# Optimization experiments

Hardware: AMD Instinct MI355X
Metric: run time of the kernel (lower is better)

Reference implementation:

```python
import jax, jax.numpy as jnp
import numpy as np

E = 8
DIMS = [512, 1024, 1024, 512]
BATCH = 2048


def _init_w(key, shape):
    a = np.sqrt(6.0 / (shape[-2] * shape[-1]))
    return jax.random.uniform(key, shape, dtype=jnp.float32, minval=-a, maxval=a)


def setup_inputs() -> dict:
    key = jax.random.key(0)
    ks = jax.random.split(key, 8)
    inp = {
        "weight_blend": jax.random.uniform(ks[0], (BATCH, E), dtype=jnp.float32),
        "x": jax.random.normal(ks[1], (BATCH, DIMS[0]), dtype=jnp.float32),
    }
    for i in range(3):
        inp[f"W{i}"] = _init_w(ks[2 + i], (E, DIMS[i + 1], DIMS[i]))
        inp[f"B{i}"] = jnp.zeros((E, DIMS[i + 1], 1), dtype=jnp.float32)
    return inp


def reference(weight_blend, x, W0, B0, W1, B1, W2, B2):
    Ws = [W0, W1, W2]
    Bs = [B0, B1, B2]
    acts = [jax.nn.elu, jax.nn.elu, None]
    for W, B, act in zip(Ws, Bs, acts):
        # dropout p=0 -> identity
        # blended-expert GEMM: sum_e wb[b,e] * (W[e] @ x[b]) == einsum
        t = jnp.einsum("be,eoi,bi->bo", weight_blend, W, x)
        bias = jnp.einsum("be,eo->bo", weight_blend, B[..., 0])
        x = t + bias
        if act is not None:
            x = act(x)
    return x
```

## Files before the change

### kernel.cpp

```cpp
#include <hip/hip_runtime.h>
#include <math.h>

typedef __attribute__((ext_vector_type(8))) short bf16x8;
typedef __attribute__((ext_vector_type(4))) float f32x4;

#define NEXP 8
#define BATCH 2048

__device__ __forceinline__ unsigned short f2bf(float f) {
    union { float f; unsigned u; } v; v.f = f;
    unsigned r = v.u + 0x7FFFu + ((v.u >> 16) & 1u);
    return (unsigned short)(r >> 16);
}

__global__ __launch_bounds__(256) void pack_all(
    const float* __restrict__ W0, const float* __restrict__ W1,
    const float* __restrict__ W2, const float* __restrict__ x,
    unsigned short* __restrict__ W0p, unsigned short* __restrict__ W1p,
    unsigned short* __restrict__ W2p, unsigned short* __restrict__ x0p)
{
    __shared__ float T[128 * 36];
    const int bid = blockIdx.x, t = threadIdx.x;

    if (bid < 10240) {
        const float* W; unsigned short* out; int KB, Din, Dout, U, lin;
        if (bid < 2048)      { W = W0; out = W0p; KB = 16; Din = 512;  Dout = 1024; U = 4; lin = bid; }
        else if (bid < 6144) { W = W1; out = W1p; KB = 32; Din = 1024; Dout = 1024; U = 4; lin = bid - 2048; }
        else                 { W = W2; out = W2p; KB = 32; Din = 1024; Dout = 512;  U = 2; lin = bid - 6144; }
        const int e  = lin & 7;
        const int r  = lin >> 3;
        const int kb = r % KB;
        const int nb = r / KB;
        const int N0 = nb * 16 * U;
        const int K0 = kb * 32;
        for (int it = 0; it < U / 2; ++it) {
            const int idx = t + 256 * it;
            const int nl = idx >> 3, k4 = (idx & 7) * 4;
            float4 v = *(const float4*)(W + ((size_t)e * Dout + N0 + nl) * Din + K0 + k4);
            *(float4*)(T + nl * 36 + k4) = v;
        }
        __syncthreads();
        if (t < 64 * U) {
            const int u = t >> 6, l = t & 63;
            const float* p = T + (u * 16 + (l & 15)) * 36 + (l >> 4) * 8;
            bf16x8 h;
            #pragma unroll
            for (int j = 0; j < 8; ++j) h[j] = (short)f2bf(p[j]);
            *(bf16x8*)(out + (size_t)lin * (U * 512) + t * 8) = h;
        }
    } else {
        const int lin = bid - 10240;
        const int kb = lin & 15, mb = lin >> 4;
        for (int it = 0; it < 4; ++it) {
            const int idx = t + 256 * it;
            const int ml = idx >> 3, k4 = (idx & 7) * 4;
            float4 v = *(const float4*)(x + (size_t)(mb * 128 + ml) * 512 + kb * 32 + k4);
            *(float4*)(T + ml * 36 + k4) = v;
        }
        __syncthreads();
        #pragma unroll
        for (int it = 0; it < 2; ++it) {
            const int s = t + 256 * it;
            const int g = s >> 6, l = s & 63;
            const float* p = T + (g * 16 + (l & 15)) * 36 + (l >> 4) * 8;
            bf16x8 h;
            #pragma unroll
            for (int j = 0; j < 8; ++j) h[j] = (short)f2bf(p[j]);
            *(bf16x8*)(x0p + (size_t)lin * 4096 + s * 8) = h;
        }
    }
}

template<int NU>
__global__ __launch_bounds__(512, 2) void moe_mfma5(
    const unsigned short* __restrict__ Xp,
    const unsigned short* __restrict__ Wp,
    const float* __restrict__ Bias,
    const float* __restrict__ WBl,
    void* __restrict__ Yout,
    int KB, int Dout, int KBn, int act, int packed_out)
{
    constexpr int BN   = 16 * NU;
    constexpr int PSTR = BN + 4;
    __shared__ __align__(16) float lds_f[2 * 32 * PSTR];

    const int tid = threadIdx.x;
    const int w   = tid >> 6;
    const int l   = tid & 63;
    const int lh  = l >> 4;
    const int ll  = l & 15;
    const int mw  = w & 1;
    const int ew  = w >> 1;
    const int e0  = 2 * ew;
    const int by  = blockIdx.y;
    const int bx  = blockIdx.x;
    const int m0  = by * 128;
    const int n0  = bx * BN;

    f32x4 acc0[4][NU], acc1[4][NU];
    #pragma unroll
    for (int t = 0; t < 4; ++t)
        #pragma unroll
        for (int u = 0; u < NU; ++u)
            #pragma unroll
            for (int i = 0; i < 4; ++i) { acc0[t][u][i] = 0.f; acc1[t][u][i] = 0.f; }

    unsigned aoff[4], boff0[NU], boff1[NU];
    #pragma unroll
    for (int t = 0; t < 4; ++t)
        aoff[t] = ((unsigned)(by * KB) * 8 + mw * 4 + t) * 1024u + l * 16u;
    #pragma unroll
    for (int u = 0; u < NU; ++u) {
        boff0[u] = ((unsigned)(bx * KB) * (8 * NU) + e0 * NU + u) * 1024u + l * 16u;
        boff1[u] = boff0[u] + NU * 1024u;
    }
    const char* xc = (const char*)Xp;
    const char* wc = (const char*)Wp;

    bf16x8 aR[2][4], b0R[2][NU], b1R[2][NU];

    auto LOAD = [&](int s, int kk) {
        const unsigned ab = (unsigned)kk * 8192u;
        const unsigned bb = (unsigned)kk * (8192u * NU);
        #pragma unroll
        for (int t = 0; t < 4; ++t)
            aR[s][t] = *(const bf16x8*)(xc + aoff[t] + ab);
        #pragma unroll
        for (int u = 0; u < NU; ++u) {
            b0R[s][u] = *(const bf16x8*)(wc + boff0[u] + bb);
            b1R[s][u] = *(const bf16x8*)(wc + boff1[u] + bb);
        }
    };
    auto MF = [&](int s) {
        #pragma unroll
        for (int u = 0; u < NU; ++u)
            #pragma unroll
            for (int t = 0; t < 4; ++t) {
                acc0[t][u] = __builtin_amdgcn_mfma_f32_16x16x32_bf16(aR[s][t], b0R[s][u], acc0[t][u], 0, 0, 0);
                acc1[t][u] = __builtin_amdgcn_mfma_f32_16x16x32_bf16(aR[s][t], b1R[s][u], acc1[t][u], 0, 0, 0);
            }
    };

    LOAD(0, 0);
    for (int kk = 0; kk < KB; kk += 2) {
        if (kk + 1 < KB) LOAD(1, kk + 1);
        MF(0);
        if (kk + 2 < KB) LOAD(0, kk + 2);
        MF(1);
    }

    float bi0[NU], bi1[NU];
    #pragma unroll
    for (int u = 0; u < NU; ++u) {
        const int n = n0 + u * 16 + ll;
        bi0[u] = Bias[(size_t)e0 * Dout + n];
        bi1[u] = Bias[(size_t)(e0 + 1) * Dout + n];
    }

    float* pb0 = lds_f;
    float* pb1 = lds_f + 32 * PSTR;
    float* pb  = (ew & 2) ? pb1 : pb0;

    #pragma unroll
    for (int tc = 0; tc < 4; ++tc) {
        __syncthreads();
        if (!(ew & 1)) {
            #pragma unroll
            for (int r = 0; r < 4; ++r) {
                const int lm = 16 * mw + 4 * lh + r;
                const int m  = m0 + 64 * mw + 16 * tc + 4 * lh + r;
                float2 wbp = ((const float2*)(WBl + (size_t)m * NEXP))[ew];
                #pragma unroll
                for (int u = 0; u < NU; ++u)
                    pb[lm * PSTR + u * 16 + ll] =
                        wbp.x * (acc0[tc][u][r] + bi0[u]) + wbp.y * (acc1[tc][u][r] + bi1[u]);
            }
        }
        __syncthreads();
        if (ew & 1) {
            #pragma unroll
            for (int r = 0; r < 4; ++r) {
                const int lm = 16 * mw + 4 * lh + r;
                const int m  = m0 + 64 * mw + 16 * tc + 4 * lh + r;
                float2 wbp = ((const float2*)(WBl + (size_t)m * NEXP))[ew];
                #pragma unroll
                for (int u = 0; u < NU; ++u)
                    pb[lm * PSTR + u * 16 + ll] +=
                        wbp.x * (acc0[tc][u][r] + bi0[u]) + wbp.y * (acc1[tc][u][r] + bi1[u]);
            }
        }
        __syncthreads();
        if (packed_out) {
            const int s = tid;
            if (s < NU * 64) {
                const int kb_loc = s >> 7;
                const int mwq    = (s >> 6) & 1;
                const int sl     = s & 63;
                const int lm     = mwq * 16 + (sl & 15);
                const int c0     = kb_loc * 32 + (sl >> 4) * 8;
                bf16x8 h;
                #pragma unroll
                for (int j = 0; j < 8; ++j) {
                    float v = pb0[lm * PSTR + c0 + j] + pb1[lm * PSTR + c0 + j];
                    v = v > 0.f ? v : expm1f(v);
                    h[j] = (short)f2bf(v);
                }
                const unsigned dst =
                    (((unsigned)by * KBn + (n0 >> 5) + kb_loc) * 8 + mwq * 4 + tc) * 1024u
                    + (unsigned)sl * 16u;
                *(bf16x8*)((char*)Yout + dst) = h;
            }
        } else {
            for (int idx = tid; idx < 32 * BN / 4; idx += 512) {
                const int row = idx / (BN / 4);
                const int c4  = (idx % (BN / 4)) * 4;
                float4 sv = *(const float4*)(pb0 + row * PSTR + c4);
                float4 qv = *(const float4*)(pb1 + row * PSTR + c4);
                sv.x += qv.x; sv.y += qv.y; sv.z += qv.z; sv.w += qv.w;
                if (act) {
                    sv.x = sv.x > 0.f ? sv.x : expm1f(sv.x);
                    sv.y = sv.y > 0.f ? sv.y : expm1f(sv.y);
                    sv.z = sv.z > 0.f ? sv.z : expm1f(sv.z);
                    sv.w = sv.w > 0.f ? sv.w : expm1f(sv.w);
                }
                const int m = m0 + 64 * (row >> 4) + 16 * tc + (row & 15);
                *(float4*)((float*)Yout + (size_t)m * Dout + n0 + c4) = sv;
            }
        }
    }
}

#define BM 64
#define BNF 64
#define BKF 16
#define PAD 4

__global__ __launch_bounds__(256) void moe_layer_f32(
    const float* __restrict__ X, const float* __restrict__ W,
    const float* __restrict__ Bias, const float* __restrict__ WB,
    float* __restrict__ Y, int Din, int Dout, int act)
{
    __shared__ float As[BKF][BM + PAD];
    __shared__ float Bs[BKF][BNF + PAD];
    const int tid = threadIdx.x;
    const int tm = tid >> 4, tn = tid & 15;
    const int m0 = blockIdx.y * BM, n0 = blockIdx.x * BNF;
    const int lr = tid >> 2, lc = (tid & 3) << 2;
    float acc[4][4] = {};
    const float* xrow  = X  + (size_t)(m0 + lr) * Din;
    const float* wbrow = WB + (size_t)(m0 + lr) * NEXP;
    const float* wrow0 = W  + (size_t)(n0 + lr) * Din;
    for (int e = 0; e < NEXP; ++e) {
        const float wbe = wbrow[e];
        const float* wrow = wrow0 + (size_t)e * Dout * Din;
        for (int k0 = 0; k0 < Din; k0 += BKF) {
            float4 av = *(const float4*)(xrow + k0 + lc);
            float4 bv = *(const float4*)(wrow + k0 + lc);
            __syncthreads();
            As[lc+0][lr] = av.x*wbe; As[lc+1][lr] = av.y*wbe;
            As[lc+2][lr] = av.z*wbe; As[lc+3][lr] = av.w*wbe;
            Bs[lc+0][lr] = bv.x; Bs[lc+1][lr] = bv.y;
            Bs[lc+2][lr] = bv.z; Bs[lc+3][lr] = bv.w;
            __syncthreads();
            #pragma unroll
            for (int k = 0; k < BKF; ++k) {
                float4 a = *(const float4*)&As[k][tm << 2];
                float4 b = *(const float4*)&Bs[k][tn << 2];
                acc[0][0]+=a.x*b.x; acc[0][1]+=a.x*b.y; acc[0][2]+=a.x*b.z; acc[0][3]+=a.x*b.w;
                acc[1][0]+=a.y*b.x; acc[1][1]+=a.y*b.y; acc[1][2]+=a.y*b.z; acc[1][3]+=a.y*b.w;
                acc[2][0]+=a.z*b.x; acc[2][1]+=a.z*b.y; acc[2][2]+=a.z*b.z; acc[2][3]+=a.z*b.w;
                acc[3][0]+=a.w*b.x; acc[3][1]+=a.w*b.y; acc[3][2]+=a.w*b.z; acc[3][3]+=a.w*b.w;
            }
        }
    }
    #pragma unroll
    for (int im = 0; im < 4; ++im) {
        const int m = m0 + (tm << 2) + im;
        const float* wbm = WB + (size_t)m * NEXP;
        float wv[NEXP];
        #pragma unroll
        for (int e = 0; e < NEXP; ++e) wv[e] = wbm[e];
        #pragma unroll
        for (int in = 0; in < 4; ++in) {
            const int n = n0 + (tn << 2) + in;
            float bsum = 0.f;
            #pragma unroll
            for (int e = 0; e < NEXP; ++e) bsum += wv[e] * Bias[(size_t)e * Dout + n];
            float v = acc[im][in] + bsum;
            if (act) v = v > 0.f ? v : expm1f(v);
            acc[im][in] = v;
        }
        float4 o = make_float4(acc[im][0], acc[im][1], acc[im][2], acc[im][3]);
        *(float4*)(Y + (size_t)m * Dout + n0 + (tn << 2)) = o;
    }
}

extern "C" void kernel_launch(void* const* d_in, const int* in_sizes, int n_in,
                              void* d_out, int out_size, void* d_ws, size_t ws_size,
                              hipStream_t stream)
{
    (void)in_sizes; (void)n_in; (void)out_size;
    const float* wb = (const float*)d_in[0];
    const float* x  = (const float*)d_in[1];
    const float* W0 = (const float*)d_in[2];
    const float* B0 = (const float*)d_in[3];
    const float* W1 = (const float*)d_in[4];
    const float* B1 = (const float*)d_in[5];
    const float* W2 = (const float*)d_in[6];
    const float* B2 = (const float*)d_in[7];
    float* out = (float*)d_out;

    const size_t NW0 = (size_t)8*1024*512, NW1 = (size_t)8*1024*1024, NW2 = (size_t)8*512*1024;
    const size_t NX0 = (size_t)BATCH*512, NX1 = (size_t)BATCH*1024;
    const size_t need = (NW0 + NW1 + NW2 + NX0 + 2 * NX1) * 2;

    if (ws_size >= need) {
        unsigned short* W0p = (unsigned short*)d_ws;
        unsigned short* W1p = W0p + NW0;
        unsigned short* W2p = W1p + NW1;
        unsigned short* x0p = W2p + NW2;
        unsigned short* x1p = x0p + NX0;
        unsigned short* x2p = x1p + NX1;
        pack_all<<<10496, 256, 0, stream>>>(W0, W1, W2, x, W0p, W1p, W2p, x0p);
        moe_mfma5<4><<<dim3(16, 16), 512, 0, stream>>>(x0p, W0p, B0, wb, x1p, 16, 1024, 32, 1, 1);
        moe_mfma5<4><<<dim3(16, 16), 512, 0, stream>>>(x1p, W1p, B1, wb, x2p, 32, 1024, 32, 1, 1);
        moe_mfma5<2><<<dim3(16, 16), 512, 0, stream>>>(x2p, W2p, B2, wb, out, 32, 512,  0, 0, 0);
    } else {
        float* x1 = (float*)d_ws;
        float* x2 = x1 + (size_t)BATCH * 1024;
        moe_layer_f32<<<dim3(1024/BNF, BATCH/BM), 256, 0, stream>>>(x,  W0, B0, wb, x1, 512,  1024, 1);
        moe_layer_f32<<<dim3(1024/BNF, BATCH/BM), 256, 0, stream>>>(x1, W1, B1, wb, x2, 1024, 1024, 1);
        moe_layer_f32<<<dim3(512/BNF,  BATCH/BM), 256, 0, stream>>>(x2, W2, B2, wb, out, 1024, 512,  0);
    }
}
```

Baseline: 202.3 us.

## Shrink MFMA GEMM tiles to 64x32 with 256 threads for more blocks

Replaces the 512-thread, 128xBN-tile blended-expert GEMM kernel with a 256-thread kernel that computes 64x32 output tiles, each wave owning two experts across all rows. This quadruples the grid (1024 blocks for the 1024-wide layers) so more CUs are busy, and collapses the four-pass LDS reduction epilogue into one two-phase pass. The trade-off is less reuse of each loaded weight and activation fragment per block, so more global/L2 traffic per FLOP.

```diff
diff --git a/kernel.cpp b/kernel.cpp
--- a/kernel.cpp
+++ b/kernel.cpp
@@ -71,8 +71,8 @@
     }
 }
 
-template<int NU>
-__global__ __launch_bounds__(512, 2) void moe_mfma5(
+template<int UP>
+__global__ __launch_bounds__(256, 3) void moe_mfma6(
     const unsigned short* __restrict__ Xp,
     const unsigned short* __restrict__ Wp,
     const float* __restrict__ Bias,
@@ -80,60 +80,64 @@
     void* __restrict__ Yout,
     int KB, int Dout, int KBn, int act, int packed_out)
 {
-    constexpr int BN   = 16 * NU;
-    constexpr int PSTR = BN + 4;
-    __shared__ __align__(16) float lds_f[2 * 32 * PSTR];
-
-    const int tid = threadIdx.x;
-    const int w   = tid >> 6;
-    const int l   = tid & 63;
-    const int lh  = l >> 4;
-    const int ll  = l & 15;
-    const int mw  = w & 1;
-    const int ew  = w >> 1;
-    const int e0  = 2 * ew;
-    const int by  = blockIdx.y;
-    const int bx  = blockIdx.x;
-    const int m0  = by * 128;
-    const int n0  = bx * BN;
-
-    f32x4 acc0[4][NU], acc1[4][NU];
+    constexpr int PSTR = 36;
+    __shared__ __align__(16) float lds_f[2 * 64 * PSTR];
+
+    const int tid  = threadIdx.x;
+    const int ew   = tid >> 6;
+    const int l    = tid & 63;
+    const int lh   = l >> 4;
+    const int ll   = l & 15;
+    const int e0   = 2 * ew;
+    const int bx   = blockIdx.x;
+    const int by   = blockIdx.y;
+    const int m0   = by * 64;
+    const int n0   = bx * 32;
+    const int mb   = by >> 1;
+    const int half = by & 1;
+
+    f32x4 acc0[4][2], acc1[4][2];
     #pragma unroll
     for (int t = 0; t < 4; ++t)
         #pragma unroll
-        for (int u = 0; u < NU; ++u)
+        for (int u = 0; u < 2; ++u)
             #pragma unroll
             for (int i = 0; i < 4; ++i) { acc0[t][u][i] = 0.f; acc1[t][u][i] = 0.f; }
 
-    unsigned aoff[4], boff0[NU], boff1[NU];
+    unsigned aoff[4];
     #pragma unroll
     for (int t = 0; t < 4; ++t)
-        aoff[t] = ((unsigned)(by * KB) * 8 + mw * 4 + t) * 1024u + l * 16u;
-    #pragma unroll
-    for (int u = 0; u < NU; ++u) {
-        boff0[u] = ((unsigned)(bx * KB) * (8 * NU) + e0 * NU + u) * 1024u + l * 16u;
-        boff1[u] = boff0[u] + NU * 1024u;
-    }
+        aoff[t] = (unsigned)(mb * KB) * 8192u + (unsigned)(half * 4 + t) * 1024u + l * 16u;
+    const int nb   = (bx * 2) / UP;
+    const int uoff = (bx * 2) % UP;
+    unsigned boff0[2], boff1[2];
+    #pragma unroll
+    for (int u = 0; u < 2; ++u) {
+        boff0[u] = (((unsigned)(nb * KB) * 8 + e0) * UP + uoff + u) * 1024u + l * 16u;
+        boff1[u] = boff0[u] + UP * 1024u;
+    }
+    const unsigned astr = 8192u;
+    const unsigned bstr = UP * 8192u;
     const char* xc = (const char*)Xp;
     const char* wc = (const char*)Wp;
 
-    bf16x8 aR[2][4], b0R[2][NU], b1R[2][NU];
+    bf16x8 aR[2][4], b0R[2][2], b1R[2][2];
 
     auto LOAD = [&](int s, int kk) {
-        const unsigned ab = (unsigned)kk * 8192u;
-        const unsigned bb = (unsigned)kk * (8192u * NU);
+        const unsigned ab = (unsigned)kk * astr;
+        const unsigned bb = (unsigned)kk * bstr;
         #pragma unroll
         for (int t = 0; t < 4; ++t)
             aR[s][t] = *(const bf16x8*)(xc + aoff[t] + ab);
         #pragma unroll
-        for (int u = 0; u < NU; ++u) {
+        for (int u = 0; u < 2; ++u) {
             b0R[s][u] = *(const bf16x8*)(wc + boff0[u] + bb);
             b1R[s][u] = *(const bf16x8*)(wc + boff1[u] + bb);
         }
     };
     auto MF = [&](int s) {
         #pragma unroll
-        for (int u = 0; u < NU; ++u)
+        for (int u = 0; u < 2; ++u)
             #pragma unroll
             for (int t = 0; t < 4; ++t) {
                 acc0[t][u] = __builtin_amdgcn_mfma_f32_16x16x32_bf16(aR[s][t], b0R[s][u], acc0[t][u], 0, 0, 0);
@@ -149,83 +153,77 @@
         MF(1);
     }
 
-    float bi0[NU], bi1[NU];
-    #pragma unroll
-    for (int u = 0; u < NU; ++u) {
+    float bi0[2], bi1[2];
+    #pragma unroll
+    for (int u = 0; u < 2; ++u) {
         const int n = n0 + u * 16 + ll;
         bi0[u] = Bias[(size_t)e0 * Dout + n];
         bi1[u] = Bias[(size_t)(e0 + 1) * Dout + n];
     }
 
+    float* pb = lds_f + (ew & 1) * (64 * PSTR);
+
+    if (ew < 2) {
+        #pragma unroll
+        for (int t = 0; t < 4; ++t)
+            #pragma unroll
+            for (int r = 0; r < 4; ++r) {
+                const int lm = 16 * t + 4 * lh + r;
+                float2 wbp = ((const float2*)(WBl + (size_t)(m0 + lm) * NEXP))[ew];
+                #pragma unroll
+                for (int u = 0; u < 2; ++u)
+                    pb[lm * PSTR + u * 16 + ll] =
+                        wbp.x * (acc0[t][u][r] + bi0[u]) + wbp.y * (acc1[t][u][r] + bi1[u]);
+            }
+    }
+    __syncthreads();
+    if (ew >= 2) {
+        #pragma unroll
+        for (int t = 0; t < 4; ++t)
+            #pragma unroll
+            for (int r = 0; r < 4; ++r) {
+                const int lm = 16 * t + 4 * lh + r;
+                float2 wbp = ((const float2*)(WBl + (size_t)(m0 + lm) * NEXP))[ew];
+                #pragma unroll
+                for (int u = 0; u < 2; ++u)
+                    pb[lm * PSTR + u * 16 + ll] +=
+                        wbp.x * (acc0[t][u][r] + bi0[u]) + wbp.y * (acc1[t][u][r] + bi1[u]);
+            }
+    }
+    __syncthreads();
+
     float* pb0 = lds_f;
-    float* pb1 = lds_f + 32 * PSTR;
-    float* pb  = (ew & 2) ? pb1 : pb0;
-
-    #pragma unroll
-    for (int tc = 0; tc < 4; ++tc) {
-        __syncthreads();
-        if (!(ew & 1)) {
-            #pragma unroll
-            for (int r = 0; r < 4; ++r) {
-                const int lm = 16 * mw + 4 * lh + r;
-                const int m  = m0 + 64 * mw + 16 * tc + 4 * lh + r;
-                float2 wbp = ((const float2*)(WBl + (size_t)m * NEXP))[ew];
-                #pragma unroll
-                for (int u = 0; u < NU; ++u)
-                    pb[lm * PSTR + u * 16 + ll] =
-                        wbp.x * (acc0[tc][u][r] + bi0[u]) + wbp.y * (acc1[tc][u][r] + bi1[u]);
-            }
-        }
-        __syncthreads();
-        if (ew & 1) {
-            #pragma unroll
-            for (int r = 0; r < 4; ++r) {
-                const int lm = 16 * mw + 4 * lh + r;
-                const int m  = m0 + 64 * mw + 16 * tc + 4 * lh + r;
-                float2 wbp = ((const float2*)(WBl + (size_t)m * NEXP))[ew];
-                #pragma unroll
-                for (int u = 0; u < NU; ++u)
-                    pb[lm * PSTR + u * 16 + ll] +=
-                        wbp.x * (acc0[tc][u][r] + bi0[u]) + wbp.y * (acc1[tc][u][r] + bi1[u]);
-            }
-        }
-        __syncthreads();
-        if (packed_out) {
-            const int s = tid;
-            if (s < NU * 64) {
-                const int kb_loc = s >> 7;
-                const int mwq    = (s >> 6) & 1;
-                const int sl     = s & 63;
-                const int lm     = mwq * 16 + (sl & 15);
-                const int c0     = kb_loc * 32 + (sl >> 4) * 8;
-                bf16x8 h;
-                #pragma unroll
-                for (int j = 0; j < 8; ++j) {
-                    float v = pb0[lm * PSTR + c0 + j] + pb1[lm * PSTR + c0 + j];
-                    v = v > 0.f ? v : expm1f(v);
-                    h[j] = (short)f2bf(v);
-                }
-                const unsigned dst =
-                    (((unsigned)by * KBn + (n0 >> 5) + kb_loc) * 8 + mwq * 4 + tc) * 1024u
-                    + (unsigned)sl * 16u;
-                *(bf16x8*)((char*)Yout + dst) = h;
-            }
-        } else {
-            for (int idx = tid; idx < 32 * BN / 4; idx += 512) {
-                const int row = idx / (BN / 4);
-                const int c4  = (idx % (BN / 4)) * 4;
-                float4 sv = *(const float4*)(pb0 + row * PSTR + c4);
-                float4 qv = *(const float4*)(pb1 + row * PSTR + c4);
-                sv.x += qv.x; sv.y += qv.y; sv.z += qv.z; sv.w += qv.w;
-                if (act) {
-                    sv.x = sv.x > 0.f ? sv.x : expm1f(sv.x);
-                    sv.y = sv.y > 0.f ? sv.y : expm1f(sv.y);
-                    sv.z = sv.z > 0.f ? sv.z : expm1f(sv.z);
-                    sv.w = sv.w > 0.f ? sv.w : expm1f(sv.w);
-                }
-                const int m = m0 + 64 * (row >> 4) + 16 * tc + (row & 15);
-                *(float4*)((float*)Yout + (size_t)m * Dout + n0 + c4) = sv;
-            }
+    float* pb1 = lds_f + 64 * PSTR;
+    if (packed_out) {
+        const int g  = tid >> 6;
+        const int c0 = lh * 8;
+        const int rowbase = (g * 16 + ll) * PSTR;
+        bf16x8 h;
+        #pragma unroll
+        for (int j = 0; j < 8; ++j) {
+            float v = pb0[rowbase + c0 + j] + pb1[rowbase + c0 + j];
+            if (act) v = v > 0.f ? v : expm1f(v);
+            h[j] = (short)f2bf(v);
+        }
+        unsigned short* dst = (unsigned short*)Yout +
+            ((size_t)(mb * KBn + bx) * 8 + half * 4 + g) * 512 + l * 8;
+        *(bf16x8*)dst = h;
+    } else {
+        #pragma unroll
+        for (int it = 0; it < 2; ++it) {
+            const int idx = tid + 256 * it;
+            const int row = idx >> 3;
+            const int c4  = (idx & 7) * 4;
+            float4 s = *(const float4*)(pb0 + row * PSTR + c4);
+            float4 q = *(const float4*)(pb1 + row * PSTR + c4);
+            s.x += q.x; s.y += q.y; s.z += q.z; s.w += q.w;
+            if (act) {
+                s.x = s.x > 0.f ? s.x : expm1f(s.x);
+                s.y = s.y > 0.f ? s.y : expm1f(s.y);
+                s.z = s.z > 0.f ? s.z : expm1f(s.z);
+                s.w = s.w > 0.f ? s.w : expm1f(s.w);
+            }
+            *(float4*)((float*)Yout + (size_t)(m0 + row) * Dout + n0 + c4) = s;
         }
     }
 }
@@ -322,9 +320,9 @@
         unsigned short* x1p = x0p + NX0;
         unsigned short* x2p = x1p + NX1;
         pack_all<<<10496, 256, 0, stream>>>(W0, W1, W2, x, W0p, W1p, W2p, x0p);
-        moe_mfma5<4><<<dim3(16, 16), 512, 0, stream>>>(x0p, W0p, B0, wb, x1p, 16, 1024, 32, 1, 1);
-        moe_mfma5<4><<<dim3(16, 16), 512, 0, stream>>>(x1p, W1p, B1, wb, x2p, 32, 1024, 32, 1, 1);
-        moe_mfma5<2><<<dim3(16, 16), 512, 0, stream>>>(x2p, W2p, B2, wb, out, 32, 512,  0, 0, 0);
+        moe_mfma6<4><<<dim3(32, 32), 256, 0, stream>>>(x0p, W0p, B0, wb, x1p, 16, 1024, 32, 1, 1);
+        moe_mfma6<4><<<dim3(32, 32), 256, 0, stream>>>(x1p, W1p, B1, wb, x2p, 32, 1024, 32, 1, 1);
+        moe_mfma6<2><<<dim3(16, 32), 256, 0, stream>>>(x2p, W2p, B2, wb, out, 32, 512,  0, 0, 0);
     } else {
         float* x1 = (float*)d_ws;
         float* x2 = x1 + (size_t)BATCH * 1024;
```

Result: no change. 201.8 us (-0.3%).
